# Kernel tuning notes

Hardware: AMD Instinct MI355X
Metric: run time of the kernel (lower is better)

## Reference

```python
import jax, jax.numpy as jnp
import numpy as np

B, L, C = 2048, 2048, 16
F = L // 2                 # num_freqs = 1024
H = 4 * F                  # multi_factor * num_freqs = 4096
P = int(len(np.unique(L // np.arange(1, F + 1))))  # n patch sizes = 88
SCALE = 0.02
NOISE_EPS = 0.01


def setup_inputs() -> dict:
    key = jax.random.key(0)
    ks = jax.random.split(key, 10)
    return {
        "x": jax.random.normal(ks[0], (B, L, C), jnp.float32),
        "w_start": SCALE * jax.random.normal(ks[1], (C, 1), jnp.float32),
        "b_start": SCALE * jax.random.normal(ks[2], (1,), jnp.float32),
        "w1": SCALE * jax.random.normal(ks[3], (2, F, H), jnp.float32),
        "b1": SCALE * jax.random.normal(ks[4], (2, H), jnp.float32),
        "w2": SCALE * jax.random.normal(ks[5], (2, H, F), jnp.float32),
        "b2": SCALE * jax.random.normal(ks[6], (2, F), jnp.float32),
        "w_gate": SCALE * jax.random.normal(ks[7], (F, P), jnp.float32),
        "w_noise": SCALE * jax.random.normal(ks[8], (F, P), jnp.float32),
        "noise_z": jax.random.normal(ks[9], (B, P), jnp.float32),
        "top_k": 3,
    }


def reference(x, w_start, b_start, w1, b1, w2, b2, w_gate, w_noise, noise_z, top_k):
    # start_fc: [B, L, C] -> [B, L, 1] -> [B, 1, L]
    v = (jnp.einsum("blc,co->blo", x, w_start) + b_start).transpose(0, 2, 1)
    # rfft (ortho), drop DC bin -> [B, 1, F] complex
    xf = jnp.fft.rfft(v, axis=-1, norm="ortho")[:, :, 1:]
    xr, xi = jnp.real(xf), jnp.imag(xf)
    # complex 2-layer MLP in frequency domain
    o1r = jax.nn.relu(jnp.einsum("bdi,io->bdo", xr, w1[0]) - jnp.einsum("bdi,io->bdo", xi, w1[1]) + b1[0])
    o1i = jax.nn.relu(jnp.einsum("bdi,io->bdo", xi, w1[0]) + jnp.einsum("bdi,io->bdo", xr, w1[1]) + b1[1])
    o2r = jnp.einsum("bdo,of->bdf", o1r, w2[0]) - jnp.einsum("bdo,of->bdf", o1i, w2[1]) + b2[0]
    o2i = jnp.einsum("bdo,of->bdf", o1i, w2[0]) + jnp.einsum("bdo,of->bdf", o1r, w2[1]) + b2[1]
    amp = jnp.sqrt(o2r * o2r + o2i * o2i)[:, 0, :]  # [B, F]
    # router logits with (training) noise injection
    clean_logits = amp @ w_gate                      # [B, P]
    noise_std = jax.nn.softplus(amp @ w_noise) + NOISE_EPS
    logits = clean_logits + noise_z * noise_std
    # top-k -> softmax over top-k -> scatter into sparse gates
    top_w, top_i = jax.lax.top_k(logits, top_k)
    top_w = jax.nn.softmax(top_w, axis=-1)
    rows = jnp.arange(logits.shape[0])[:, None]
    gates = jnp.zeros_like(logits).at[rows, top_i].set(top_w)
    return gates
```

## Files before the change

kernel.cpp:

```cpp
#include <hip/hip_runtime.h>
#include <hip/hip_bf16.h>
#include <math.h>

#define B_DIM 2048
#define L_DIM 2048
#define F_DIM 1024
#define H_DIM 4096
#define P_DIM 88

typedef unsigned short u16;
typedef short bf16x8 __attribute__((ext_vector_type(8)));
typedef float f32x4 __attribute__((ext_vector_type(4)));

__device__ __forceinline__ u16 f2bf(float x) {
    unsigned u = __float_as_uint(x);
    return (u16)((u + 0x7fffu + ((u >> 16) & 1u)) >> 16);
}
__device__ __forceinline__ float bf2f(u16 h) {
    return __uint_as_float(((unsigned)h) << 16);
}

__device__ __forceinline__ void gload_lds16(const void* g, void* l) {
    unsigned loff = (unsigned)(uintptr_t)l;
    __builtin_amdgcn_global_load_lds(
        reinterpret_cast<const __attribute__((address_space(1))) void*>(
            reinterpret_cast<uintptr_t>(g)),
        reinterpret_cast<__attribute__((address_space(3))) void*>(loff),
        16, 0, 0);
}

__global__ __launch_bounds__(256) void start_fc_kernel(
    const float* __restrict__ x, const float* __restrict__ w_start,
    const float* __restrict__ b_start, float* __restrict__ v)
{
    size_t gid = (size_t)blockIdx.x * 256 + threadIdx.x;
    const float4* xp = (const float4*)(x + gid * 16);
    const float4* wp = (const float4*)w_start;
    float acc = b_start[0];
#pragma unroll
    for (int q = 0; q < 4; q++) {
        float4 xv = xp[q];
        float4 wv = wp[q];
        acc += xv.x * wv.x + xv.y * wv.y + xv.z * wv.z + xv.w * wv.w;
    }
    v[gid] = acc;
}

__global__ __launch_bounds__(256) void fft_kernel(
    const float* __restrict__ v, u16* __restrict__ A1)
{
    __shared__ float re[2048];
    __shared__ float im[2048];
    int b = blockIdx.x;
    const float* row = v + (size_t)b * 2048;

    for (int i = threadIdx.x; i < 2048; i += 256) {
        unsigned j = __brev((unsigned)i) >> 21;
        re[i] = row[j];
        im[i] = 0.f;
    }
    __syncthreads();

    for (int s = 1; s <= 11; s++) {
        int half = 1 << (s - 1);
        for (int t = threadIdx.x; t < 1024; t += 256) {
            int j = t & (half - 1);
            int base = (t >> (s - 1)) << s;
            float ang = -6.283185307179586f * (float)j / (float)(1 << s);
            float wr, wi;
            sincosf(ang, &wi, &wr);
            int i0 = base + j, i1 = i0 + half;
            float br = re[i1], bi = im[i1];
            float tr = br * wr - bi * wi;
            float ti = br * wi + bi * wr;
            float ar = re[i0], ai = im[i0];
            re[i0] = ar + tr; im[i0] = ai + ti;
            re[i1] = ar - tr; im[i1] = ai - ti;
        }
        __syncthreads();
    }

    const float sc = 0.022097086912079612f;
    u16* arow = A1 + (size_t)b * 4096;
    for (int t = threadIdx.x; t < 1024; t += 256) {
        float r = re[t + 1] * sc;
        float q = im[t + 1] * sc;
        u16 rh = f2bf(r); u16 rl = f2bf(r - bf2f(rh));
        u16 ih = f2bf(q); u16 il = f2bf(q - bf2f(ih));
        arow[t] = rh; arow[1024 + t] = rl;
        arow[2048 + t] = ih; arow[3072 + t] = il;
    }
}

__global__ __launch_bounds__(256) void conv_bt_kernel(
    const float* __restrict__ w, u16* __restrict__ BT, int Kc, int Nh)
{
    __shared__ float t0[32][33];
    __shared__ float t1[32][33];
    int k0 = blockIdx.x * 32, n0 = blockIdx.y * 32;
    int tx = threadIdx.x, ty = threadIdx.y;
    const float* w0 = w;
    const float* w1 = w + (size_t)Kc * Nh;

#pragma unroll
    for (int i = 0; i < 4; i++) {
        int k = k0 + ty + 8 * i;
        t0[ty + 8 * i][tx] = w0[(size_t)k * Nh + n0 + tx];
        t1[ty + 8 * i][tx] = w1[(size_t)k * Nh + n0 + tx];
    }
    __syncthreads();

    size_t K4 = 4 * (size_t)Kc;
    int k = k0 + tx;
#pragma unroll
    for (int i = 0; i < 4; i++) {
        int nl = ty + 8 * i;
        int n = n0 + nl;
        float br = t0[tx][nl];
        float bi = t1[tx][nl];
        u16 brh = f2bf(br); u16 brl = f2bf(br - bf2f(brh));
        float nbi = -bi;
        u16 nih = f2bf(nbi); u16 nil = f2bf(nbi - bf2f(nih));
        u16 pih = f2bf(bi);  u16 pil = f2bf(bi - bf2f(pih));
        u16* rowr = BT + (size_t)n * K4;
        rowr[0 * Kc + k] = brh; rowr[1 * Kc + k] = brl;
        rowr[2 * Kc + k] = nih; rowr[3 * Kc + k] = nil;
        u16* rowi = BT + (size_t)(Nh + n) * K4;
        rowi[0 * Kc + k] = pih; rowi[1 * Kc + k] = pil;
        rowi[2 * Kc + k] = brh; rowi[3 * Kc + k] = brl;
    }
}

extern __shared__ char smem8p[];

template <int EPI, int SWZ>
__global__ __launch_bounds__(512, 2) void gemm8p(
    const u16* __restrict__ A, const u16* __restrict__ B,
    const float* __restrict__ biasL, const float* __restrict__ biasR,
    u16* __restrict__ OutU, float* __restrict__ P01, float* __restrict__ P23,
    int Kc, int KcLog, int NH, int nt)
{
    char* ldsA = smem8p;
    char* ldsB = smem8p + 65536;

    const int tid = threadIdx.x;
    const int w = tid >> 6, lane = tid & 63;
    const int wr = w >> 2, wc = w & 3;
    const int fr = lane & 15, kb = lane >> 4;

    int bx, by, z;
    if (SWZ) {
        int b = blockIdx.x;
        int xcd = b & 7, idx = b >> 3;
        bx = 4 * xcd + (idx & 3);
        by = idx >> 2;
        z = 0;
    } else {
        bx = blockIdx.x; by = blockIdx.y; z = blockIdx.z;
    }
    const int n0 = bx * 256, m0 = by * 256;
    const size_t K4 = 4 * (size_t)Kc;

    const int srow = tid >> 2;
    const int lk8 = (((tid & 3) ^ ((tid >> 3) & 3))) * 8;
    const int wb = (tid >> 6) * 1024;

    const int laneOff = fr * 64 + ((kb ^ ((fr >> 1) & 3)) << 4);

    f32x4 acc[8][4];
#pragma unroll
    for (int i = 0; i < 8; i++)
#pragma unroll
        for (int j = 0; j < 4; j++)
            acc[i][j] = (f32x4){0.f, 0.f, 0.f, 0.f};

    const int t0 = z * nt, te = t0 + nt;

    auto colA = [&](int t) {
        int k0 = t << 5;
        int seg = k0 >> KcLog, kk = k0 & (Kc - 1);
        int r3 = seg >= 3 ? seg - 3 : seg;
        int bs = seg >= 3 ? 2 : 0;
        return (bs + (r3 == 1 ? 1 : 0)) * Kc + kk;
    };
    auto colB = [&](int t) {
        int k0 = t << 5;
        int seg = k0 >> KcLog, kk = k0 & (Kc - 1);
        int r3 = seg >= 3 ? seg - 3 : seg;
        int bs = seg >= 3 ? 2 : 0;
        return (bs + (r3 == 2 ? 1 : 0)) * Kc + kk;
    };
    auto stageA = [&](int t) {
        const u16* src = A + (size_t)(m0 + srow) * K4 + colA(t) + lk8;
        char* dst = ldsA + (t & 3) * 16384 + wb;
        gload_lds16(src, dst);
        gload_lds16(src + (size_t)128 * K4, dst + 8192);
    };
    auto stageB = [&](int t) {
        const u16* src = B + (size_t)(n0 + srow) * K4 + colB(t) + lk8;
        char* dst = ldsB + (t & 3) * 16384 + wb;
        gload_lds16(src, dst);
        gload_lds16(src + (size_t)128 * K4, dst + 8192);
    };

    stageA(t0); stageB(t0);
    if (t0 + 1 < te) { stageA(t0 + 1); stageB(t0 + 1); }

    for (int t = t0; t < te; ++t) {
        if (t + 1 < te) asm volatile("s_waitcnt vmcnt(4)" ::: "memory");
        else            asm volatile("s_waitcnt vmcnt(0)" ::: "memory");
        asm volatile("s_barrier" ::: "memory");

        const int slot = t & 3;
        const char* aS = ldsA + slot * 16384 + wr * 8192 + laneOff;
        const char* bS = ldsB + slot * 16384 + wc * 4096 + laneOff;

        bf16x8 b0 = *(const bf16x8*)(bS + 0 * 1024);
        bf16x8 b1 = *(const bf16x8*)(bS + 1 * 1024);
        bf16x8 b2 = *(const bf16x8*)(bS + 2 * 1024);
        bf16x8 b3 = *(const bf16x8*)(bS + 3 * 1024);
        bf16x8 a0 = *(const bf16x8*)(aS + 0 * 1024);
        bf16x8 a1 = *(const bf16x8*)(aS + 1 * 1024);
        bf16x8 a2 = *(const bf16x8*)(aS + 2 * 1024);
        bf16x8 a3 = *(const bf16x8*)(aS + 3 * 1024);
        if (t + 2 < te) stageA(t + 2);

        __builtin_amdgcn_s_setprio(1);
        acc[0][0] = __builtin_amdgcn_mfma_f32_16x16x32_bf16(a0, b0, acc[0][0], 0, 0, 0);
        acc[0][1] = __builtin_amdgcn_mfma_f32_16x16x32_bf16(a0, b1, acc[0][1], 0, 0, 0);
        acc[0][2] = __builtin_amdgcn_mfma_f32_16x16x32_bf16(a0, b2, acc[0][2], 0, 0, 0);
        acc[0][3] = __builtin_amdgcn_mfma_f32_16x16x32_bf16(a0, b3, acc[0][3], 0, 0, 0);
        acc[1][0] = __builtin_amdgcn_mfma_f32_16x16x32_bf16(a1, b0, acc[1][0], 0, 0, 0);
        acc[1][1] = __builtin_amdgcn_mfma_f32_16x16x32_bf16(a1, b1, acc[1][1], 0, 0, 0);
        acc[1][2] = __builtin_amdgcn_mfma_f32_16x16x32_bf16(a1, b2, acc[1][2], 0, 0, 0);
        acc[1][3] = __builtin_amdgcn_mfma_f32_16x16x32_bf16(a1, b3, acc[1][3], 0, 0, 0);
        acc[2][0] = __builtin_amdgcn_mfma_f32_16x16x32_bf16(a2, b0, acc[2][0], 0, 0, 0);
        acc[2][1] = __builtin_amdgcn_mfma_f32_16x16x32_bf16(a2, b1, acc[2][1], 0, 0, 0);
        acc[2][2] = __builtin_amdgcn_mfma_f32_16x16x32_bf16(a2, b2, acc[2][2], 0, 0, 0);
        acc[2][3] = __builtin_amdgcn_mfma_f32_16x16x32_bf16(a2, b3, acc[2][3], 0, 0, 0);
        acc[3][0] = __builtin_amdgcn_mfma_f32_16x16x32_bf16(a3, b0, acc[3][0], 0, 0, 0);
        acc[3][1] = __builtin_amdgcn_mfma_f32_16x16x32_bf16(a3, b1, acc[3][1], 0, 0, 0);
        acc[3][2] = __builtin_amdgcn_mfma_f32_16x16x32_bf16(a3, b2, acc[3][2], 0, 0, 0);
        acc[3][3] = __builtin_amdgcn_mfma_f32_16x16x32_bf16(a3, b3, acc[3][3], 0, 0, 0);
        __builtin_amdgcn_s_setprio(0);
        asm volatile("s_barrier" ::: "memory");

        a0 = *(const bf16x8*)(aS + 4096 + 0 * 1024);
        a1 = *(const bf16x8*)(aS + 4096 + 1 * 1024);
        a2 = *(const bf16x8*)(aS + 4096 + 2 * 1024);
        a3 = *(const bf16x8*)(aS + 4096 + 3 * 1024);
        if (t + 2 < te) stageB(t + 2);

        __builtin_amdgcn_s_setprio(1);
        acc[4][0] = __builtin_amdgcn_mfma_f32_16x16x32_bf16(a0, b0, acc[4][0], 0, 0, 0);
        acc[4][1] = __builtin_amdgcn_mfma_f32_16x16x32_bf16(a0, b1, acc[4][1], 0, 0, 0);
        acc[4][2] = __builtin_amdgcn_mfma_f32_16x16x32_bf16(a0, b2, acc[4][2], 0, 0, 0);
        acc[4][3] = __builtin_amdgcn_mfma_f32_16x16x32_bf16(a0, b3, acc[4][3], 0, 0, 0);
        acc[5][0] = __builtin_amdgcn_mfma_f32_16x16x32_bf16(a1, b0, acc[5][0], 0, 0, 0);
        acc[5][1] = __builtin_amdgcn_mfma_f32_16x16x32_bf16(a1, b1, acc[5][1], 0, 0, 0);
        acc[5][2] = __builtin_amdgcn_mfma_f32_16x16x32_bf16(a1, b2, acc[5][2], 0, 0, 0);
        acc[5][3] = __builtin_amdgcn_mfma_f32_16x16x32_bf16(a1, b3, acc[5][3], 0, 0, 0);
        acc[6][0] = __builtin_amdgcn_mfma_f32_16x16x32_bf16(a2, b0, acc[6][0], 0, 0, 0);
        acc[6][1] = __builtin_amdgcn_mfma_f32_16x16x32_bf16(a2, b1, acc[6][1], 0, 0, 0);
        acc[6][2] = __builtin_amdgcn_mfma_f32_16x16x32_bf16(a2, b2, acc[6][2], 0, 0, 0);
        acc[6][3] = __builtin_amdgcn_mfma_f32_16x16x32_bf16(a2, b3, acc[6][3], 0, 0, 0);
        acc[7][0] = __builtin_amdgcn_mfma_f32_16x16x32_bf16(a3, b0, acc[7][0], 0, 0, 0);
        acc[7][1] = __builtin_amdgcn_mfma_f32_16x16x32_bf16(a3, b1, acc[7][1], 0, 0, 0);
        acc[7][2] = __builtin_amdgcn_mfma_f32_16x16x32_bf16(a3, b2, acc[7][2], 0, 0, 0);
        acc[7][3] = __builtin_amdgcn_mfma_f32_16x16x32_bf16(a3, b3, acc[7][3], 0, 0, 0);
        __builtin_amdgcn_s_setprio(0);
    }

    const int fq = kb;
#pragma unroll
    for (int nj = 0; nj < 4; nj++) {
        int n = n0 + wc * 64 + nj * 16 + fr;
        if (EPI == 0) {
            bool left = (n < NH);
            int nn = left ? n : (n - NH);
            float bias = left ? biasL[n] : biasR[nn];
#pragma unroll
            for (int mi = 0; mi < 8; mi++) {
                int mb = m0 + wr * 128 + mi * 16 + fq * 4;
#pragma unroll
                for (int r = 0; r < 4; r++) {
                    float val = fmaxf(acc[mi][nj][r] + bias, 0.f);
                    u16 h = f2bf(val);
                    u16 lo = f2bf(val - bf2f(h));
                    size_t rb = (size_t)(mb + r) * (4 * (size_t)NH);
                    if (left) { OutU[rb + nn] = h; OutU[rb + NH + nn] = lo; }
                    else { OutU[rb + 2 * (size_t)NH + nn] = h; OutU[rb + 3 * (size_t)NH + nn] = lo; }
                }
            }
        } else {
            const size_t PSZ = (size_t)2048 * 2048;
            float* Out = (z < 2) ? (P01 + (size_t)z * PSZ) : (P23 + (size_t)(z - 2) * PSZ);
#pragma unroll
            for (int mi = 0; mi < 8; mi++) {
                int mb = m0 + wr * 128 + mi * 16 + fq * 4;
#pragma unroll
                for (int r = 0; r < 4; r++)
                    Out[(size_t)(mb + r) * 2048 + n] = acc[mi][nj][r];
            }
        }
    }
}

__global__ __launch_bounds__(128) void router_kernel(
    const float* __restrict__ P01, const float* __restrict__ P23, int ZK,
    const float* __restrict__ b2,
    const float* __restrict__ w_gate, const float* __restrict__ w_noise,
    const float* __restrict__ noise_z, float* __restrict__ gates)
{
    __shared__ float s_amp[1024];
    __shared__ float s_logit[P_DIM];
    __shared__ int   s_idx[3];
    __shared__ float s_val[3];

    int b = blockIdx.x;
    const size_t PSZ = (size_t)2048 * 2048;
    const size_t roff = (size_t)b * 2048;

    for (int i = threadIdx.x; i < 1024; i += 128) {
        float orr = b2[i];
        float oii = b2[1024 + i];
        for (int zz = 0; zz < ZK; zz++) {
            const float* Pz = ((zz < 2) ? (P01 + (size_t)zz * PSZ)
                                        : (P23 + (size_t)(zz - 2) * PSZ)) + roff;
            orr += Pz[i];
            oii += Pz[1024 + i];
        }
        s_amp[i] = sqrtf(orr * orr + oii * oii);
    }
    __syncthreads();

    int p = threadIdx.x;
    if (p < P_DIM) {
        float cg = 0.f, cn = 0.f;
        for (int k = 0; k < 1024; k++) {
            float a = s_amp[k];
            cg = fmaf(a, w_gate[k * P_DIM + p], cg);
            cn = fmaf(a, w_noise[k * P_DIM + p], cn);
        }
        float ns = (cn > 20.f) ? cn : log1pf(expf(cn));
        ns += 0.01f;
        s_logit[p] = cg + noise_z[(size_t)b * P_DIM + p] * ns;
    }
    __syncthreads();

    if (threadIdx.x == 0) {
        int i0 = -1, i1 = -1, i2 = -1;
        float v0 = -1e30f, v1 = -1e30f, v2 = -1e30f;
        for (int i = 0; i < P_DIM; i++) {
            float t = s_logit[i];
            if (t > v0) { v0 = t; i0 = i; }
        }
        for (int i = 0; i < P_DIM; i++) {
            if (i == i0) continue;
            float t = s_logit[i];
            if (t > v1) { v1 = t; i1 = i; }
        }
        for (int i = 0; i < P_DIM; i++) {
            if (i == i0 || i == i1) continue;
            float t = s_logit[i];
            if (t > v2) { v2 = t; i2 = i; }
        }
        s_idx[0] = i0; s_idx[1] = i1; s_idx[2] = i2;
        s_val[0] = v0; s_val[1] = v1; s_val[2] = v2;
    }
    __syncthreads();

    if (p < P_DIM) {
        float m = s_val[0];
        float e0 = expf(s_val[0] - m);
        float e1 = expf(s_val[1] - m);
        float e2 = expf(s_val[2] - m);
        float inv = 1.f / (e0 + e1 + e2);
        float g = 0.f;
        if (p == s_idx[0]) g = e0 * inv;
        else if (p == s_idx[1]) g = e1 * inv;
        else if (p == s_idx[2]) g = e2 * inv;
        gates[(size_t)b * P_DIM + p] = g;
    }
}

extern "C" void kernel_launch(void* const* d_in, const int* in_sizes, int n_in,
                              void* d_out, int out_size, void* d_ws, size_t ws_size,
                              hipStream_t stream)
{
    const float* x       = (const float*)d_in[0];
    const float* w_start = (const float*)d_in[1];
    const float* b_start = (const float*)d_in[2];
    const float* w1      = (const float*)d_in[3];
    const float* b1      = (const float*)d_in[4];
    const float* w2      = (const float*)d_in[5];
    const float* b2      = (const float*)d_in[6];
    const float* w_gate  = (const float*)d_in[7];
    const float* w_noise = (const float*)d_in[8];
    const float* noise_z = (const float*)d_in[9];
    float* gates = (float*)d_out;

    const size_t MB = 1024 * 1024;
    char* base = (char*)d_ws;
    float* v   = (float*)base;
    u16*  A1   = (u16*)(base + 16 * MB);
    u16*  BT   = (u16*)(base + 32 * MB);
    u16*  A2   = (u16*)(base + 96 * MB);
    float* P01 = (float*)base;
    float* P23 = (float*)(base + 160 * MB);

    int ZK = (ws_size >= (size_t)192 * MB) ? 4 : 2;

    hipFuncSetAttribute(reinterpret_cast<const void*>(&gemm8p<0, 1>),
                        hipFuncAttributeMaxDynamicSharedMemorySize, 131072);
    hipFuncSetAttribute(reinterpret_cast<const void*>(&gemm8p<1, 0>),
                        hipFuncAttributeMaxDynamicSharedMemorySize, 131072);

    start_fc_kernel<<<(B_DIM * L_DIM) / 256, 256, 0, stream>>>(x, w_start, b_start, v);
    fft_kernel<<<B_DIM, 256, 0, stream>>>(v, A1);

    conv_bt_kernel<<<dim3(F_DIM / 32, H_DIM / 32), dim3(32, 8), 0, stream>>>(
        w1, BT, F_DIM, H_DIM);
    gemm8p<0, 1><<<256, 512, 131072, stream>>>(
        A1, BT, b1, b1 + H_DIM, A2, nullptr, nullptr, F_DIM, 10, H_DIM, 192);

    conv_bt_kernel<<<dim3(H_DIM / 32, F_DIM / 32), dim3(32, 8), 0, stream>>>(
        w2, BT, H_DIM, F_DIM);
    gemm8p<1, 0><<<dim3(8, 8, ZK), 512, 131072, stream>>>(
        A2, BT, nullptr, nullptr, nullptr, P01, P23, H_DIM, 12, F_DIM, 768 / ZK);

    router_kernel<<<B_DIM, 128, 0, stream>>>(
        P01, P23, ZK, b2, w_gate, w_noise, noise_z, gates);
}
```

Baseline: 633.3 us.

## Fuse start_fc into FFT and restructure GEMM main loop with register prefetch

The start_fc projection is folded into the FFT kernel, so each block reads x directly and writes bit-reversed values into shared memory, which removes the intermediate v buffer and one kernel launch. The GEMM main loop is reorganised so the A and B tiles for the next K-step are issued together at the top of the iteration. Next-step fragments are loaded from LDS into registers after the second MFMA group, and each iteration now has one barrier instead of two. This is meant to overlap LDS reads with MFMA work and cut synchronisation, at the cost of more live registers. The 4-slot ring buffer must stay safe when staging two steps ahead with fewer barriers.

```diff
diff --git a/kernel.cpp b/kernel.cpp
--- a/kernel.cpp
+++ b/kernel.cpp
@@ -29,35 +29,29 @@
         16, 0, 0);
 }
 
-__global__ __launch_bounds__(256) void start_fc_kernel(
+__global__ __launch_bounds__(256) void fft_kernel(
     const float* __restrict__ x, const float* __restrict__ w_start,
-    const float* __restrict__ b_start, float* __restrict__ v)
-{
-    size_t gid = (size_t)blockIdx.x * 256 + threadIdx.x;
-    const float4* xp = (const float4*)(x + gid * 16);
-    const float4* wp = (const float4*)w_start;
-    float acc = b_start[0];
-#pragma unroll
-    for (int q = 0; q < 4; q++) {
-        float4 xv = xp[q];
-        float4 wv = wp[q];
-        acc += xv.x * wv.x + xv.y * wv.y + xv.z * wv.z + xv.w * wv.w;
-    }
-    v[gid] = acc;
-}
-
-__global__ __launch_bounds__(256) void fft_kernel(
-    const float* __restrict__ v, u16* __restrict__ A1)
+    const float* __restrict__ b_start, u16* __restrict__ A1)
 {
     __shared__ float re[2048];
     __shared__ float im[2048];
     int b = blockIdx.x;
-    const float* row = v + (size_t)b * 2048;
-
-    for (int i = threadIdx.x; i < 2048; i += 256) {
-        unsigned j = __brev((unsigned)i) >> 21;
-        re[i] = row[j];
-        im[i] = 0.f;
+
+    const float4* wp = (const float4*)w_start;
+    float4 w0 = wp[0], w1 = wp[1], w2 = wp[2], w3 = wp[3];
+    float bs = b_start[0];
+
+    for (int l = threadIdx.x; l < 2048; l += 256) {
+        const float4* xp = (const float4*)(x + ((size_t)b * 2048 + l) * 16);
+        float4 x0 = xp[0], x1 = xp[1], x2 = xp[2], x3 = xp[3];
+        float acc = bs;
+        acc += x0.x * w0.x + x0.y * w0.y + x0.z * w0.z + x0.w * w0.w;
+        acc += x1.x * w1.x + x1.y * w1.y + x1.z * w1.z + x1.w * w1.w;
+        acc += x2.x * w2.x + x2.y * w2.y + x2.z * w2.z + x2.w * w2.w;
+        acc += x3.x * w3.x + x3.y * w3.y + x3.z * w3.z + x3.w * w3.w;
+        unsigned j = __brev((unsigned)l) >> 21;
+        re[j] = acc;
+        im[j] = 0.f;
     }
     __syncthreads();
 
@@ -133,6 +127,24 @@
 
 extern __shared__ char smem8p[];
 
+#define MFMA16(ACC0, ACC1, ACC2, ACC3, A0, A1, A2, A3)                          \
+    ACC0[0] = __builtin_amdgcn_mfma_f32_16x16x32_bf16(A0, b0, ACC0[0], 0, 0, 0); \
+    ACC0[1] = __builtin_amdgcn_mfma_f32_16x16x32_bf16(A0, b1, ACC0[1], 0, 0, 0); \
+    ACC0[2] = __builtin_amdgcn_mfma_f32_16x16x32_bf16(A0, b2, ACC0[2], 0, 0, 0); \
+    ACC0[3] = __builtin_amdgcn_mfma_f32_16x16x32_bf16(A0, b3, ACC0[3], 0, 0, 0); \
+    ACC1[0] = __builtin_amdgcn_mfma_f32_16x16x32_bf16(A1, b0, ACC1[0], 0, 0, 0); \
+    ACC1[1] = __builtin_amdgcn_mfma_f32_16x16x32_bf16(A1, b1, ACC1[1], 0, 0, 0); \
+    ACC1[2] = __builtin_amdgcn_mfma_f32_16x16x32_bf16(A1, b2, ACC1[2], 0, 0, 0); \
+    ACC1[3] = __builtin_amdgcn_mfma_f32_16x16x32_bf16(A1, b3, ACC1[3], 0, 0, 0); \
+    ACC2[0] = __builtin_amdgcn_mfma_f32_16x16x32_bf16(A2, b0, ACC2[0], 0, 0, 0); \
+    ACC2[1] = __builtin_amdgcn_mfma_f32_16x16x32_bf16(A2, b1, ACC2[1], 0, 0, 0); \
+    ACC2[2] = __builtin_amdgcn_mfma_f32_16x16x32_bf16(A2, b2, ACC2[2], 0, 0, 0); \
+    ACC2[3] = __builtin_amdgcn_mfma_f32_16x16x32_bf16(A2, b3, ACC2[3], 0, 0, 0); \
+    ACC3[0] = __builtin_amdgcn_mfma_f32_16x16x32_bf16(A3, b0, ACC3[0], 0, 0, 0); \
+    ACC3[1] = __builtin_amdgcn_mfma_f32_16x16x32_bf16(A3, b1, ACC3[1], 0, 0, 0); \
+    ACC3[2] = __builtin_amdgcn_mfma_f32_16x16x32_bf16(A3, b2, ACC3[2], 0, 0, 0); \
+    ACC3[3] = __builtin_amdgcn_mfma_f32_16x16x32_bf16(A3, b3, ACC3[3], 0, 0, 0);
+
 template <int EPI, int SWZ>
 __global__ __launch_bounds__(512, 2) void gemm8p(
     const u16* __restrict__ A, const u16* __restrict__ B,
@@ -202,73 +214,66 @@
         gload_lds16(src, dst);
         gload_lds16(src + (size_t)128 * K4, dst + 8192);
     };
+    auto aBase = [&](int t) -> const char* {
+        return ldsA + (t & 3) * 16384 + wr * 8192 + laneOff;
+    };
+    auto bBase = [&](int t) -> const char* {
+        return ldsB + (t & 3) * 16384 + wc * 4096 + laneOff;
+    };
 
     stageA(t0); stageB(t0);
     if (t0 + 1 < te) { stageA(t0 + 1); stageB(t0 + 1); }
+    if (t0 + 1 < te) asm volatile("s_waitcnt vmcnt(4)" ::: "memory");
+    else             asm volatile("s_waitcnt vmcnt(0)" ::: "memory");
+    asm volatile("s_barrier" ::: "memory");
+
+    bf16x8 b0, b1, b2, b3, a0, a1, a2, a3;
+    {
+        const char* aS = aBase(t0);
+        const char* bS = bBase(t0);
+        b0 = *(const bf16x8*)(bS + 0 * 1024);
+        b1 = *(const bf16x8*)(bS + 1 * 1024);
+        b2 = *(const bf16x8*)(bS + 2 * 1024);
+        b3 = *(const bf16x8*)(bS + 3 * 1024);
+        a0 = *(const bf16x8*)(aS + 0 * 1024);
+        a1 = *(const bf16x8*)(aS + 1 * 1024);
+        a2 = *(const bf16x8*)(aS + 2 * 1024);
+        a3 = *(const bf16x8*)(aS + 3 * 1024);
+    }
 
     for (int t = t0; t < te; ++t) {
-        if (t + 1 < te) asm volatile("s_waitcnt vmcnt(4)" ::: "memory");
+        if (t + 2 < te) { stageA(t + 2); stageB(t + 2); }
+
+        __builtin_amdgcn_s_setprio(1);
+        MFMA16(acc[0], acc[1], acc[2], acc[3], a0, a1, a2, a3)
+        __builtin_amdgcn_s_setprio(0);
+
+        const char* aS = aBase(t);
+        bf16x8 c0 = *(const bf16x8*)(aS + 4096 + 0 * 1024);
+        bf16x8 c1 = *(const bf16x8*)(aS + 4096 + 1 * 1024);
+        bf16x8 c2 = *(const bf16x8*)(aS + 4096 + 2 * 1024);
+        bf16x8 c3 = *(const bf16x8*)(aS + 4096 + 3 * 1024);
+
+        if (t + 2 < te) asm volatile("s_waitcnt vmcnt(4)" ::: "memory");
         else            asm volatile("s_waitcnt vmcnt(0)" ::: "memory");
         asm volatile("s_barrier" ::: "memory");
 
-        const int slot = t & 3;
-        const char* aS = ldsA + slot * 16384 + wr * 8192 + laneOff;
-        const char* bS = ldsB + slot * 16384 + wc * 4096 + laneOff;
-
-        bf16x8 b0 = *(const bf16x8*)(bS + 0 * 1024);
-        bf16x8 b1 = *(const bf16x8*)(bS + 1 * 1024);
-        bf16x8 b2 = *(const bf16x8*)(bS + 2 * 1024);
-        bf16x8 b3 = *(const bf16x8*)(bS + 3 * 1024);
-        bf16x8 a0 = *(const bf16x8*)(aS + 0 * 1024);
-        bf16x8 a1 = *(const bf16x8*)(aS + 1 * 1024);
-        bf16x8 a2 = *(const bf16x8*)(aS + 2 * 1024);
-        bf16x8 a3 = *(const bf16x8*)(aS + 3 * 1024);
-        if (t + 2 < te) stageA(t + 2);
-
         __builtin_amdgcn_s_setprio(1);
-        acc[0][0] = __builtin_amdgcn_mfma_f32_16x16x32_bf16(a0, b0, acc[0][0], 0, 0, 0);
-        acc[0][1] = __builtin_amdgcn_mfma_f32_16x16x32_bf16(a0, b1, acc[0][1], 0, 0, 0);
-        acc[0][2] = __builtin_amdgcn_mfma_f32_16x16x32_bf16(a0, b2, acc[0][2], 0, 0, 0);
-        acc[0][3] = __builtin_amdgcn_mfma_f32_16x16x32_bf16(a0, b3, acc[0][3], 0, 0, 0);
-        acc[1][0] = __builtin_amdgcn_mfma_f32_16x16x32_bf16(a1, b0, acc[1][0], 0, 0, 0);
-        acc[1][1] = __builtin_amdgcn_mfma_f32_16x16x32_bf16(a1, b1, acc[1][1], 0, 0, 0);
-        acc[1][2] = __builtin_amdgcn_mfma_f32_16x16x32_bf16(a1, b2, acc[1][2], 0, 0, 0);
-        acc[1][3] = __builtin_amdgcn_mfma_f32_16x16x32_bf16(a1, b3, acc[1][3], 0, 0, 0);
-        acc[2][0] = __builtin_amdgcn_mfma_f32_16x16x32_bf16(a2, b0, acc[2][0], 0, 0, 0);
-        acc[2][1] = __builtin_amdgcn_mfma_f32_16x16x32_bf16(a2, b1, acc[2][1], 0, 0, 0);
-        acc[2][2] = __builtin_amdgcn_mfma_f32_16x16x32_bf16(a2, b2, acc[2][2], 0, 0, 0);
-        acc[2][3] = __builtin_amdgcn_mfma_f32_16x16x32_bf16(a2, b3, acc[2][3], 0, 0, 0);
-        acc[3][0] = __builtin_amdgcn_mfma_f32_16x16x32_bf16(a3, b0, acc[3][0], 0, 0, 0);
-        acc[3][1] = __builtin_amdgcn_mfma_f32_16x16x32_bf16(a3, b1, acc[3][1], 0, 0, 0);
-        acc[3][2] = __builtin_amdgcn_mfma_f32_16x16x32_bf16(a3, b2, acc[3][2], 0, 0, 0);
-        acc[3][3] = __builtin_amdgcn_mfma_f32_16x16x32_bf16(a3, b3, acc[3][3], 0, 0, 0);
+        MFMA16(acc[4], acc[5], acc[6], acc[7], c0, c1, c2, c3)
         __builtin_amdgcn_s_setprio(0);
-        asm volatile("s_barrier" ::: "memory");
-
-        a0 = *(const bf16x8*)(aS + 4096 + 0 * 1024);
-        a1 = *(const bf16x8*)(aS + 4096 + 1 * 1024);
-        a2 = *(const bf16x8*)(aS + 4096 + 2 * 1024);
-        a3 = *(const bf16x8*)(aS + 4096 + 3 * 1024);
-        if (t + 2 < te) stageB(t + 2);
-
-        __builtin_amdgcn_s_setprio(1);
-        acc[4][0] = __builtin_amdgcn_mfma_f32_16x16x32_bf16(a0, b0, acc[4][0], 0, 0, 0);
-        acc[4][1] = __builtin_amdgcn_mfma_f32_16x16x32_bf16(a0, b1, acc[4][1], 0, 0, 0);
-        acc[4][2] = __builtin_amdgcn_mfma_f32_16x16x32_bf16(a0, b2, acc[4][2], 0, 0, 0);
-        acc[4][3] = __builtin_amdgcn_mfma_f32_16x16x32_bf16(a0, b3, acc[4][3], 0, 0, 0);
-        acc[5][0] = __builtin_amdgcn_mfma_f32_16x16x32_bf16(a1, b0, acc[5][0], 0, 0, 0);
-        acc[5][1] = __builtin_amdgcn_mfma_f32_16x16x32_bf16(a1, b1, acc[5][1], 0, 0, 0);
-        acc[5][2] = __builtin_amdgcn_mfma_f32_16x16x32_bf16(a1, b2, acc[5][2], 0, 0, 0);
-        acc[5][3] = __builtin_amdgcn_mfma_f32_16x16x32_bf16(a1, b3, acc[5][3], 0, 0, 0);
-        acc[6][0] = __builtin_amdgcn_mfma_f32_16x16x32_bf16(a2, b0, acc[6][0], 0, 0, 0);
-        acc[6][1] = __builtin_amdgcn_mfma_f32_16x16x32_bf16(a2, b1, acc[6][1], 0, 0, 0);
-        acc[6][2] = __builtin_amdgcn_mfma_f32_16x16x32_bf16(a2, b2, acc[6][2], 0, 0, 0);
-        acc[6][3] = __builtin_amdgcn_mfma_f32_16x16x32_bf16(a2, b3, acc[6][3], 0, 0, 0);
-        acc[7][0] = __builtin_amdgcn_mfma_f32_16x16x32_bf16(a3, b0, acc[7][0], 0, 0, 0);
-        acc[7][1] = __builtin_amdgcn_mfma_f32_16x16x32_bf16(a3, b1, acc[7][1], 0, 0, 0);
-        acc[7][2] = __builtin_amdgcn_mfma_f32_16x16x32_bf16(a3, b2, acc[7][2], 0, 0, 0);
-        acc[7][3] = __builtin_amdgcn_mfma_f32_16x16x32_bf16(a3, b3, acc[7][3], 0, 0, 0);
-        __builtin_amdgcn_s_setprio(0);
+
+        if (t + 1 < te) {
+            const char* aN = aBase(t + 1);
+            const char* bN = bBase(t + 1);
+            b0 = *(const bf16x8*)(bN + 0 * 1024);
+            b1 = *(const bf16x8*)(bN + 1 * 1024);
+            b2 = *(const bf16x8*)(bN + 2 * 1024);
+            b3 = *(const bf16x8*)(bN + 3 * 1024);
+            a0 = *(const bf16x8*)(aN + 0 * 1024);
+            a1 = *(const bf16x8*)(aN + 1 * 1024);
+            a2 = *(const bf16x8*)(aN + 2 * 1024);
+            a3 = *(const bf16x8*)(aN + 3 * 1024);
+        }
     }
 
     const int fq = kb;
@@ -402,7 +407,6 @@
 
     const size_t MB = 1024 * 1024;
     char* base = (char*)d_ws;
-    float* v   = (float*)base;
     u16*  A1   = (u16*)(base + 16 * MB);
     u16*  BT   = (u16*)(base + 32 * MB);
     u16*  A2   = (u16*)(base + 96 * MB);
@@ -416,8 +420,7 @@
     hipFuncSetAttribute(reinterpret_cast<const void*>(&gemm8p<1, 0>),
                         hipFuncAttributeMaxDynamicSharedMemorySize, 131072);
 
-    start_fc_kernel<<<(B_DIM * L_DIM) / 256, 256, 0, stream>>>(x, w_start, b_start, v);
-    fft_kernel<<<B_DIM, 256, 0, stream>>>(v, A1);
+    fft_kernel<<<B_DIM, 256, 0, stream>>>(x, w_start, b_start, A1);
 
     conv_bt_kernel<<<dim3(F_DIM / 32, H_DIM / 32), dim3(32, 8), 0, stream>>>(
         w1, BT, F_DIM, H_DIM);
```

After: 595.5 us. 1.06x faster.
